# Kernel optimization log

Hardware: AMD Instinct MI355X
Metric: run time of the kernel (lower is better)

Reference implementation:

```python
import jax, jax.numpy as jnp
import numpy as np

D_STATE = 16
D_CONV = 4
EXPAND = 2
GROUPS = 8
EPS = 1e-5


def _layernorm(x, w, b):
    m = x.mean(-1, keepdims=True)
    v = x.var(-1, keepdims=True)
    return (x - m) * jax.lax.rsqrt(v + EPS) * w + b


def _groupnorm(x, w, b):
    B, C = x.shape[:2]
    sp = x.shape[2:]
    xg = x.reshape(B, GROUPS, C // GROUPS, -1)
    m = xg.mean(axis=(2, 3), keepdims=True)
    v = xg.var(axis=(2, 3), keepdims=True)
    xg = (xg - m) * jax.lax.rsqrt(v + EPS)
    x = xg.reshape((B, C) + sp)
    shp = (1, C) + (1,) * len(sp)
    return x * w.reshape(shp) + b.reshape(shp)


def _mamba(xn, in_w, conv_w, conv_b, xp_w, dt_w, dt_b, A_log, Dp, out_w):
    # xn: [B, L, C]
    B, L, C = xn.shape
    di = in_w.shape[0] // 2
    rank = dt_w.shape[1]
    N = D_STATE
    xz = xn @ in_w.T                              # [B, L, 2*di]
    xi, z = xz[..., :di], xz[..., di:]
    # causal depthwise conv1d along L (pad left d_conv-1, truncate to L)
    xc = jnp.moveaxis(xi, 1, 2)                   # [B, di, L]
    xpd = jnp.pad(xc, ((0, 0), (0, 0), (D_CONV - 1, 0)))
    conv = conv_b[None, :, None]
    for k in range(D_CONV):
        conv = conv + conv_w[None, :, k, None] * xpd[:, :, k:k + L]
    u = jnp.moveaxis(jax.nn.silu(conv), 1, 2)     # [B, L, di]
    dbl = u @ xp_w.T                              # [B, L, rank+2N]
    dt = dbl[..., :rank]
    Bm = dbl[..., rank:rank + N]
    Cm = dbl[..., rank + N:]
    delta = jax.nn.softplus(dt @ dt_w.T + dt_b)   # [B, L, di]
    A = -jnp.exp(A_log)                           # [di, N]
    dA = jnp.exp(delta[..., None] * A)            # [B, L, di, N]
    dBu = delta[..., None] * Bm[:, :, None, :] * u[..., None]

    def comb(e1, e2):
        a1, b1 = e1
        a2, b2 = e2
        return a1 * a2, a2 * b1 + b2

    _, h = jax.lax.associative_scan(comb, (dA, dBu), axis=1)  # h_t = dA_t*h_{t-1} + dBu_t
    y = jnp.einsum('bldn,bln->bld', h, Cm) + u * Dp
    y = y * jax.nn.silu(z)
    return y @ out_w.T


def _mamba_layer(x, p):
    B, C = x.shape[:2]
    img = x.shape[2:]
    L = int(np.prod(img))
    xf = jnp.moveaxis(x.reshape(B, C, L), 1, 2)   # [B, L, C]
    xn = _layernorm(xf, p['ln_w'], p['ln_b'])
    xm = _mamba(xn, p['in_w'], p['conv_w'], p['conv_b'], p['xp_w'],
                p['dt_w'], p['dt_b'], p['A_log'], p['Dp'], p['out_w'])
    xm = xm + p['skip'] * xf
    xm = _layernorm(xm, p['ln_w'], p['ln_b'])     # same norm params reused, as in source
    y = xm @ p['proj_w'].T + p['proj_b']
    return jnp.moveaxis(y, 1, 2).reshape((B, C) + img)


def setup_inputs() -> dict:
    key = jax.random.key(0)
    B, C = 2, 48
    img = (16, 32, 32)
    di = EXPAND * C
    rank = -(-C // 16)
    ks = iter(jax.random.split(key, 64))

    def nrm(shape, scale):
        return jax.random.normal(next(ks), shape, jnp.float32) * scale

    inp = {'x': jax.random.normal(next(ks), (B, C) + img, jnp.float32)}
    inp['gn1_w'] = jnp.ones(C); inp['gn1_b'] = jnp.zeros(C)
    inp['gn2_w'] = jnp.ones(C); inp['gn2_b'] = jnp.zeros(C)
    for i in (1, 2):
        inp[f'ln{i}_w'] = jnp.ones(C); inp[f'ln{i}_b'] = jnp.zeros(C)
        inp[f'in_w{i}'] = nrm((2 * di, C), C ** -0.5)
        inp[f'conv_w{i}'] = nrm((di, D_CONV), D_CONV ** -0.5)
        inp[f'conv_b{i}'] = jnp.zeros(di)
        inp[f'xp_w{i}'] = nrm((rank + 2 * D_STATE, di), di ** -0.5)
        inp[f'dt_w{i}'] = nrm((di, rank), rank ** -0.5)
        inp[f'dt_b{i}'] = nrm((di,), 0.1) - 4.0  # softplus -> small positive dt
        inp[f'A_log{i}'] = jnp.log(jnp.tile(jnp.arange(1, D_STATE + 1, dtype=jnp.float32), (di, 1)))
        inp[f'D{i}'] = jnp.ones(di)
        inp[f'out_w{i}'] = nrm((C, di), di ** -0.5)
        inp[f'proj_w{i}'] = nrm((C, C), C ** -0.5)
        inp[f'proj_b{i}'] = jnp.zeros(C)
        inp[f'skip{i}'] = jnp.ones(1)
    return inp


def reference(x, gn1_w, gn1_b, gn2_w, gn2_b,
              ln1_w, ln1_b, in_w1, conv_w1, conv_b1, xp_w1, dt_w1, dt_b1, A_log1, D1, out_w1, proj_w1, proj_b1, skip1,
              ln2_w, ln2_b, in_w2, conv_w2, conv_b2, xp_w2, dt_w2, dt_b2, A_log2, D2, out_w2, proj_w2, proj_b2, skip2):
    p1 = dict(ln_w=ln1_w, ln_b=ln1_b, in_w=in_w1, conv_w=conv_w1, conv_b=conv_b1, xp_w=xp_w1,
              dt_w=dt_w1, dt_b=dt_b1, A_log=A_log1, Dp=D1, out_w=out_w1, proj_w=proj_w1,
              proj_b=proj_b1, skip=skip1)
    p2 = dict(ln_w=ln2_w, ln_b=ln2_b, in_w=in_w2, conv_w=conv_w2, conv_b=conv_b2, xp_w=xp_w2,
              dt_w=dt_w2, dt_b=dt_b2, A_log=A_log2, Dp=D2, out_w=out_w2, proj_w=proj_w2,
              proj_b=proj_b2, skip=skip2)
    identity = x
    h = jax.nn.relu(_groupnorm(x, gn1_w, gn1_b))
    h = _mamba_layer(h, p1)
    h = jax.nn.relu(_groupnorm(h, gn2_w, gn2_b))
    h = _mamba_layer(h, p2)
    return h + identity
```

## Files before the change

### kernel.cpp

```cpp
#include <hip/hip_runtime.h>
#include <hip/hip_bf16.h>

#define LCH   48
#define DI    96
#define LSEQ  16384
#define NB    2
#define NPOS  (NB*LSEQ)
#define NSTATE 16
#define CPG   6
#define EPS   1e-5f
#define NC    128
#define CL    128
#define NCHAIN (NB*DI*NSTATE)
#define TS    32
#define TSS   36
#define LOG2E 1.442695040888963f

typedef __hip_bfloat16 bf16;

__device__ __forceinline__ float LDW(const void* p, size_t i, bool f32){
    return f32 ? ((const float*)p)[i] : __bfloat162float(((const bf16*)p)[i]);
}

__device__ __forceinline__ float bf2f(unsigned short h){
    union { unsigned int i; float f; } u; u.i = ((unsigned int)h) << 16; return u.f;
}

__device__ __forceinline__ float4 LDW4(const void* p, size_t i4, bool f32){
    if (f32) return ((const float4*)p)[i4];
    ushort4 v = ((const ushort4*)p)[i4];
    return make_float4(bf2f(v.x), bf2f(v.y), bf2f(v.z), bf2f(v.w));
}

__device__ __forceinline__ float row16_sum(float p){
    union { float f; int i; } u, v;
    u.f = p; v.i = __builtin_amdgcn_mov_dpp(u.i, 0x111, 0xf, 0xf, true); p += v.f;
    u.f = p; v.i = __builtin_amdgcn_mov_dpp(u.i, 0x112, 0xf, 0xf, true); p += v.f;
    u.f = p; v.i = __builtin_amdgcn_mov_dpp(u.i, 0x114, 0xf, 0xf, true); p += v.f;
    u.f = p; v.i = __builtin_amdgcn_mov_dpp(u.i, 0x118, 0xf, 0xf, true); p += v.f;
    return p;
}

__global__ void k_flag(const void* gnw, int* flag, float* __restrict__ acc1, float* __restrict__ acc2){
    int t = threadIdx.x;
    if (t == 0){
        const unsigned short* g = (const unsigned short*)gnw;
        flag[0] = (g[0] == 0x3F80) ? 0 : 1;
    }
    if (t < 32){ acc1[t] = 0.f; acc2[t] = 0.f; }
}

__global__ void k_gnpart_x(const void* __restrict__ x, const int* Fg, float* __restrict__ acc){
    const bool f32 = Fg[0];
    int bg = blockIdx.x >> 4, sl = blockIdx.x & 15;
    int b = bg >> 3, g = bg & 7;
    int tid = threadIdx.x;
    float s = 0.f, q = 0.f;
    for (int c = 0; c < CPG; ++c){
        size_t base = (size_t)(b*LCH + g*CPG + c)*LSEQ + sl*1024;
        float4 v = LDW4(x, base/4 + tid, f32);
        s += v.x; q += v.x*v.x;
        s += v.y; q += v.y*v.y;
        s += v.z; q += v.z*v.z;
        s += v.w; q += v.w*v.w;
    }
    __shared__ float ss[256], sq[256];
    ss[tid] = s; sq[tid] = q; __syncthreads();
    for (int st = 128; st > 0; st >>= 1){
        if (tid < st){ ss[tid] += ss[tid+st]; sq[tid] += sq[tid+st]; }
        __syncthreads();
    }
    if (tid == 0){
        atomicAdd(&acc[bg*2],   ss[0]);
        atomicAdd(&acc[bg*2+1], sq[0]);
    }
}

template<int SRC>
__global__ void k_prepin(const void* __restrict__ src, const int* Fg, const float* __restrict__ acc,
                         const void* gnw, const void* gnb, const void* lnw, const void* lnb,
                         const void* __restrict__ inw,
                         float* __restrict__ xf, float* __restrict__ xi, float* __restrict__ z){
    const bool f32 = Fg[0];
    __shared__ float wl[96*52];
    __shared__ float xl[32*52];
    __shared__ float fl[32*52];
    __shared__ float sst[32];
    int tid = threadIdx.x;
    int part = blockIdx.x & 1;
    int pos0 = (blockIdx.x >> 1)*32;
    int b = pos0 >> 14, l0 = pos0 & (LSEQ-1);
    if (tid < 16){
        float mean = acc[tid*2] / (float)(CPG*LSEQ);
        float var  = acc[tid*2+1] / (float)(CPG*LSEQ) - mean*mean;
        sst[tid*2]   = mean;
        sst[tid*2+1] = rsqrtf(var + EPS);
    }
    for (int i = tid; i < 96*12; i += 256){
        int o = i/12, k4 = i - o*12;
        ((float4*)wl)[o*13+k4] = LDW4(inw, (size_t)part*1152 + i, f32);
    }
    if (SRC == 0){
        for (int i = tid; i < 48*32; i += 256){
            int c = i >> 5, p = i & 31;
            xl[p*52+c] = LDW(src, (size_t)(b*LCH+c)*LSEQ + l0 + p, f32);
        }
    } else {
        const float4* ms4 = (const float4*)src;
        for (int i = tid; i < 32*12; i += 256){
            int p = i/12, c4 = i - p*12;
            ((float4*)xl)[p*13+c4] = ms4[(size_t)pos0*12 + i];
        }
    }
    __syncthreads();
    {
        int row = tid >> 3, q = tid & 7;
        float* rrow = xl + row*52;
        float* frow = fl + row*52;
        float gmean = sst[(b*8+q)*2], grs = sst[(b*8+q)*2+1];
        float vv[6];
        float s = 0.f, qq = 0.f;
        #pragma unroll
        for (int j = 0; j < 6; ++j){
            int c = q*6 + j;
            float v = rrow[c];
            v = (v - gmean)*grs*LDW(gnw,c,f32) + LDW(gnb,c,f32);
            v = fmaxf(v, 0.f);
            vv[j] = v; frow[c] = v; s += v; qq += v*v;
        }
        s  += __shfl_xor(s, 1);  qq += __shfl_xor(qq, 1);
        s  += __shfl_xor(s, 2);  qq += __shfl_xor(qq, 2);
        s  += __shfl_xor(s, 4);  qq += __shfl_xor(qq, 4);
        float mean = s / (float)LCH;
        float rs = rsqrtf(qq/(float)LCH - mean*mean + EPS);
        #pragma unroll
        for (int j = 0; j < 6; ++j){
            int c = q*6 + j;
            rrow[c] = (vv[j]-mean)*rs*LDW(lnw,c,f32) + LDW(lnb,c,f32);
        }
    }
    __syncthreads();
    if (part == 0){
        float4* xf4 = (float4*)xf;
        const float4* fl4 = (const float4*)fl;
        for (int i = tid; i < 32*12; i += 256){
            int p = i/12, c4 = i - p*12;
            xf4[(size_t)pos0*12 + i] = fl4[p*13+c4];
        }
    }
    float* dst = part ? z : xi;
    int o  = tid & 31;
    int pg = tid >> 5;
    const float4* wl4 = (const float4*)wl;
    const float4* xl4 = (const float4*)xl;
    float a0[4] = {0.f,0.f,0.f,0.f};
    float a1[4] = {0.f,0.f,0.f,0.f};
    float a2[4] = {0.f,0.f,0.f,0.f};
    #pragma unroll
    for (int k4 = 0; k4 < 12; ++k4){
        float4 w0 = wl4[ o     *13 + k4];
        float4 w1 = wl4[(o+32)*13 + k4];
        float4 w2 = wl4[(o+64)*13 + k4];
        #pragma unroll
        for (int q = 0; q < 4; ++q){
            float4 xv = xl4[(pg*4+q)*13 + k4];
            a0[q] += xv.x*w0.x; a0[q] += xv.y*w0.y; a0[q] += xv.z*w0.z; a0[q] += xv.w*w0.w;
            a1[q] += xv.x*w1.x; a1[q] += xv.y*w1.y; a1[q] += xv.z*w1.z; a1[q] += xv.w*w1.w;
            a2[q] += xv.x*w2.x; a2[q] += xv.y*w2.y; a2[q] += xv.z*w2.z; a2[q] += xv.w*w2.w;
        }
    }
    #pragma unroll
    for (int q = 0; q < 4; ++q){
        size_t pos = (size_t)(pos0 + pg*4 + q);
        dst[pos*DI + o     ] = a0[q];
        dst[pos*DI + o + 32] = a1[q];
        dst[pos*DI + o + 64] = a2[q];
    }
}

__global__ void k_convdbl(const float* __restrict__ xi, const void* cw, const void* cb,
                          const void* __restrict__ xpw, const void* dtw, const void* dtb,
                          const int* Fg, float* __restrict__ u_g, float* __restrict__ B2,
                          float* __restrict__ C2, float* __restrict__ delta_g){
    const bool f32 = Fg[0];
    __shared__ float xil[35*100];
    __shared__ float wbc[32*100];
    __shared__ float wdt[3*100];
    __shared__ float cwl[96*4];
    __shared__ float cbl[96];
    __shared__ float dtwl[96*3];
    __shared__ float dtbl[96];
    __shared__ float dtl[32*3];
    int tid = threadIdx.x;
    int pos0 = blockIdx.x*32;
    int l0 = pos0 & (LSEQ-1);

    for (int i = tid; i < 32*24; i += 256){
        int o = i/24, k4 = i - o*24;
        int row = (o & 1) ? (19 + (o>>1)) : (3 + (o>>1));
        ((float4*)wbc)[o*25 + k4] = LDW4(xpw, (size_t)row*24 + k4, f32);
    }
    if (tid < 72){
        int o = tid/24, k4 = tid - o*24;
        ((float4*)wdt)[o*25 + k4] = LDW4(xpw, (size_t)o*24 + k4, f32);
    }
    for (int i = tid; i < 96*4; i += 256) cwl[i] = LDW(cw, i, f32);
    if (tid < 96) cbl[tid] = LDW(cb, tid, f32);
    for (int i = tid; i < 96*3; i += 256) dtwl[i] = LDW(dtw, i, f32);
    if (tid >= 128 && tid < 224) dtbl[tid-128] = LDW(dtb, tid-128, f32);
    {
        float4* xv = (float4*)xil;
        const float4* gx = (const float4*)xi;
        for (int i = tid; i < 35*24; i += 256){
            int p = i/24, k4 = i - p*24;
            float4 v = make_float4(0.f, 0.f, 0.f, 0.f);
            if (l0 + p - 3 >= 0) v = gx[(size_t)(pos0-3+p)*24 + k4];
            xv[p*25 + k4] = v;
        }
    }
    __syncthreads();

    float uu[12];
    #pragma unroll
    for (int r = 0; r < 12; ++r){
        int i = tid + 256*r;
        int j = i/96, d = i - j*96;
        float4 cw4 = ((const float4*)cwl)[d];
        float acc = cbl[d];
        acc += cw4.x*xil[(j+0)*100+d];
        acc += cw4.y*xil[(j+1)*100+d];
        acc += cw4.z*xil[(j+2)*100+d];
        acc += cw4.w*xil[(j+3)*100+d];
        uu[r] = acc / (1.f + __expf(-acc));
    }
    __syncthreads();

    #pragma unroll
    for (int r = 0; r < 12; ++r){
        int i = tid + 256*r;
        int j = i/96, d = i - j*96;
        xil[j*100+d] = uu[r];
        u_g[(size_t)pos0*DI + i] = uu[r];
    }
    __syncthreads();

    {
        int o  = tid & 31;
        int pg = ((tid>>6)<<1) | ((tid>>5)&1);
        const float4* ulv = (const float4*)xil;
        const float4* wv  = (const float4*)wbc;
        float a0=0.f, a1=0.f, a2=0.f, a3=0.f;
        #pragma unroll 4
        for (int k4 = 0; k4 < 24; ++k4){
            float4 u0 = ulv[(pg*4+0)*25 + k4];
            float4 u1 = ulv[(pg*4+1)*25 + k4];
            float4 u2 = ulv[(pg*4+2)*25 + k4];
            float4 u3 = ulv[(pg*4+3)*25 + k4];
            float4 w  = wv[o*25 + k4];
            a0 += u0.x*w.x; a0 += u0.y*w.y; a0 += u0.z*w.z; a0 += u0.w*w.w;
            a1 += u1.x*w.x; a1 += u1.y*w.y; a1 += u1.z*w.z; a1 += u1.w*w.w;
            a2 += u2.x*w.x; a2 += u2.y*w.y; a2 += u2.z*w.z; a2 += u2.w*w.w;
            a3 += u3.x*w.x; a3 += u3.y*w.y; a3 += u3.z*w.z; a3 += u3.w*w.w;
        }
        int nn = o >> 1;
        float* dst = (o & 1) ? C2 : B2;
        size_t pb = (size_t)(pos0 + pg*4);
        dst[(pb+0)*16 + nn] = a0;
        dst[(pb+1)*16 + nn] = a1;
        dst[(pb+2)*16 + nn] = a2;
        dst[(pb+3)*16 + nn] = a3;
    }
    if (tid < 96){
        int o = tid >> 5;
        int p = tid & 31;
        const float4* ulv = (const float4*)xil;
        const float4* wv  = (const float4*)wdt;
        float a = 0.f;
        #pragma unroll 4
        for (int k4 = 0; k4 < 24; ++k4){
            float4 uv = ulv[p*25 + k4];
            float4 w  = wv[o*25 + k4];
            a += uv.x*w.x; a += uv.y*w.y; a += uv.z*w.z; a += uv.w*w.w;
        }
        dtl[p*3+o] = a;
    }
    __syncthreads();

    for (int i = tid; i < 32*96; i += 256){
        int p = i/96, d = i - p*96;
        float acc = dtbl[d];
        #pragma unroll
        for (int r = 0; r < 3; ++r) acc += dtl[p*3+r]*dtwl[d*3+r];
        float sp = (acc > 20.f) ? acc : log1pf(__expf(acc));
        delta_g[(size_t)pos0*DI + i] = sp;
    }
}

__global__ void k_scanA(const float* __restrict__ delta, const float* __restrict__ u,
                        const float* __restrict__ B2, const void* Alog, const int* Fg,
                        float* __restrict__ Pb, float* __restrict__ Sb){
    const bool f32 = Fg[0];
    __shared__ float dls[2][16*TSS];
    __shared__ float uus[2][16*TSS];
    __shared__ float bbs[2][16*TSS];
    int tid = threadIdx.x;
    int t = blockIdx.x*256 + tid;
    int n = tid & 15;
    int sg0 = blockIdx.x*16;
    int cb2 = sg0/96;
    int d0 = sg0 - cb2*96;
    int b = cb2 & 1, chunk = cb2 >> 1;
    int dloc = tid >> 4;
    int d = d0 + dloc;
    float An = -__expf(LDW(Alog, d*16+n, f32)) * LOG2E;
    float P = 1.f, S = 0.f;
    int base = b*LSEQ + chunk*CL;
    int si0 = tid >> 4, sj = tid & 15;
    int si1 = si0 + 16;
    float pd0, pd1, pu0, pu1, pb0, pb1;
    auto fetch = [&](int tb){
        pd0 = delta[(size_t)(tb+si0)*DI + d0 + sj];
        pu0 = u    [(size_t)(tb+si0)*DI + d0 + sj];
        pb0 = B2   [(size_t)(tb+si0)*16 + sj];
        pd1 = delta[(size_t)(tb+si1)*DI + d0 + sj];
        pu1 = u    [(size_t)(tb+si1)*DI + d0 + sj];
        pb1 = B2   [(size_t)(tb+si1)*16 + sj];
    };
    auto store = [&](int bs){
        dls[bs][sj*TSS+si0] = pd0; dls[bs][sj*TSS+si1] = pd1;
        uus[bs][sj*TSS+si0] = pu0; uus[bs][sj*TSS+si1] = pu1;
        bbs[bs][sj*TSS+si0] = pb0; bbs[bs][sj*TSS+si1] = pb1;
    };
    fetch(base); store(0);
    __syncthreads();
    for (int tile = 0; tile < CL/TS; ++tile){
        int cur = tile & 1;
        if (tile+1 < CL/TS) fetch(base + (tile+1)*TS);
        #pragma unroll
        for (int i4 = 0; i4 < TS/4; ++i4){
            float4 dl4 = *(const float4*)&dls[cur][dloc*TSS + i4*4];
            float4 uu4 = *(const float4*)&uus[cur][dloc*TSS + i4*4];
            float4 bn4 = *(const float4*)&bbs[cur][n   *TSS + i4*4];
            float a;
            a = exp2f(dl4.x*An); P *= a; S = a*S + dl4.x*bn4.x*uu4.x;
            a = exp2f(dl4.y*An); P *= a; S = a*S + dl4.y*bn4.y*uu4.y;
            a = exp2f(dl4.z*An); P *= a; S = a*S + dl4.z*bn4.z*uu4.z;
            a = exp2f(dl4.w*An); P *= a; S = a*S + dl4.w*bn4.w*uu4.w;
        }
        if (tile+1 < CL/TS) store(1-cur);
        __syncthreads();
    }
    Pb[t] = P; Sb[t] = S;
}

__global__ void k_scanB(const float* __restrict__ Pb, const float* __restrict__ Sb,
                        float* __restrict__ carry){
    int ch = blockIdx.x*blockDim.x + threadIdx.x;
    float c = 0.f;
    for (int cb = 0; cb < NC; cb += 8){
        float P[8], S[8];
        #pragma unroll
        for (int j = 0; j < 8; ++j){
            P[j] = Pb[(size_t)(cb+j)*NCHAIN + ch];
            S[j] = Sb[(size_t)(cb+j)*NCHAIN + ch];
        }
        #pragma unroll
        for (int j = 0; j < 8; ++j){
            carry[(size_t)(cb+j)*NCHAIN + ch] = c;
            c = S[j] + P[j]*c;
        }
    }
}

__global__ void k_scanC(const float* __restrict__ delta, const float* __restrict__ u,
                        const float* __restrict__ B2, const float* __restrict__ C2,
                        const float* __restrict__ carry, const void* Alog, const void* Dp,
                        const int* Fg, float* __restrict__ y){
    const bool f32 = Fg[0];
    __shared__ float dls[2][16*TSS];
    __shared__ float uus[2][16*TSS];
    __shared__ float bbs[2][16*TSS];
    __shared__ float ccs[2][16*TSS];
    int tid = threadIdx.x;
    int n = tid & 15;
    int sg0 = blockIdx.x*16;
    int cb2 = sg0/96;
    int d0 = sg0 - cb2*96;
    int b = cb2 & 1, chunk = cb2 >> 1;
    int dloc = tid >> 4;
    int d = d0 + dloc;
    float An = -__expf(LDW(Alog, d*16+n, f32)) * LOG2E;
    float Dpd = LDW(Dp, d, f32);
    float h = carry[chunk*NCHAIN + (b*DI+d)*NSTATE + n];
    int base = b*LSEQ + chunk*CL;
    int si0 = tid >> 4, sj = tid & 15;
    int si1 = si0 + 16;
    float pd0, pd1, pu0, pu1, pb0, pb1, pc0, pc1;
    auto fetch = [&](int tb){
        pd0 = delta[(size_t)(tb+si0)*DI + d0 + sj];
        pu0 = u    [(size_t)(tb+si0)*DI + d0 + sj];
        pb0 = B2   [(size_t)(tb+si0)*16 + sj];
        pc0 = C2   [(size_t)(tb+si0)*16 + sj];
        pd1 = delta[(size_t)(tb+si1)*DI + d0 + sj];
        pu1 = u    [(size_t)(tb+si1)*DI + d0 + sj];
        pb1 = B2   [(size_t)(tb+si1)*16 + sj];
        pc1 = C2   [(size_t)(tb+si1)*16 + sj];
    };
    auto store = [&](int bs){
        dls[bs][sj*TSS+si0] = pd0; dls[bs][sj*TSS+si1] = pd1;
        uus[bs][sj*TSS+si0] = pu0; uus[bs][sj*TSS+si1] = pu1;
        bbs[bs][sj*TSS+si0] = pb0; bbs[bs][sj*TSS+si1] = pb1;
        ccs[bs][sj*TSS+si0] = pc0; ccs[bs][sj*TSS+si1] = pc1;
    };
    fetch(base); store(0);
    __syncthreads();
    for (int tile = 0; tile < CL/TS; ++tile){
        int cur = tile & 1;
        int tb = base + tile*TS;
        if (tile+1 < CL/TS) fetch(base + (tile+1)*TS);
        #pragma unroll
        for (int i4 = 0; i4 < TS/4; ++i4){
            float4 dl4 = *(const float4*)&dls[cur][dloc*TSS + i4*4];
            float4 uu4 = *(const float4*)&uus[cur][dloc*TSS + i4*4];
            float4 bn4 = *(const float4*)&bbs[cur][n   *TSS + i4*4];
            float4 cn4 = *(const float4*)&ccs[cur][n   *TSS + i4*4];
            float a, p;
            a = exp2f(dl4.x*An); h = a*h + dl4.x*bn4.x*uu4.x;
            p = row16_sum(h*cn4.x);
            if (n == 15) y[(size_t)(tb+i4*4+0)*DI + d] = p + uu4.x*Dpd;
            a = exp2f(dl4.y*An); h = a*h + dl4.y*bn4.y*uu4.y;
            p = row16_sum(h*cn4.y);
            if (n == 15) y[(size_t)(tb+i4*4+1)*DI + d] = p + uu4.y*Dpd;
            a = exp2f(dl4.z*An); h = a*h + dl4.z*bn4.z*uu4.z;
            p = row16_sum(h*cn4.z);
            if (n == 15) y[(size_t)(tb+i4*4+2)*DI + d] = p + uu4.z*Dpd;
            a = exp2f(dl4.w*An); h = a*h + dl4.w*bn4.w*uu4.w;
            p = row16_sum(h*cn4.w);
            if (n == 15) y[(size_t)(tb+i4*4+3)*DI + d] = p + uu4.w*Dpd;
        }
        if (tile+1 < CL/TS) store(1-cur);
        __syncthreads();
    }
}

__global__ void k_outproj(const float* __restrict__ psum, const void* __restrict__ outw,
                          const void* skipv, const int* Fg,
                          const float* __restrict__ zx,
                          const float* __restrict__ xf, float* __restrict__ xm){
    const bool f32 = Fg[0];
    __shared__ float wl[48*100];
    __shared__ float yl[32*100];
    int tid = threadIdx.x;
    int pos0 = blockIdx.x*32;
    for (int i = tid; i < 48*24; i += 256){
        int o = i/24, k4 = i - o*24;
        ((float4*)wl)[o*25+k4] = LDW4(outw, i, f32);
    }
    {
        const float4* ps4 = (const float4*)psum;
        const float4* zz4 = (const float4*)zx;
        for (int i = tid; i < 32*24; i += 256){
            int p = i/24, k4 = i - p*24;
            float4 pv = ps4[(size_t)pos0*24 + i];
            float4 zv = zz4[(size_t)pos0*24 + i];
            float4 y;
            y.x = pv.x * (zv.x / (1.f + __expf(-zv.x)));
            y.y = pv.y * (zv.y / (1.f + __expf(-zv.y)));
            y.z = pv.z * (zv.z / (1.f + __expf(-zv.z)));
            y.w = pv.w * (zv.w / (1.f + __expf(-zv.w)));
            ((float4*)yl)[p*25+k4] = y;
        }
    }
    __syncthreads();
    float sk = LDW(skipv, 0, f32);
    int o16 = tid & 15;
    int pg  = tid >> 4;
    const float4* wl4 = (const float4*)wl;
    const float4* yl4 = (const float4*)yl;
    float a[3][2] = {{0.f,0.f},{0.f,0.f},{0.f,0.f}};
    #pragma unroll 4
    for (int k4 = 0; k4 < 24; ++k4){
        float4 w0 = wl4[ o16     *25+k4];
        float4 w1 = wl4[(o16+16)*25+k4];
        float4 w2 = wl4[(o16+32)*25+k4];
        float4 y0 = yl4[(pg*2+0)*25+k4];
        float4 y1 = yl4[(pg*2+1)*25+k4];
        a[0][0] += y0.x*w0.x; a[0][0] += y0.y*w0.y; a[0][0] += y0.z*w0.z; a[0][0] += y0.w*w0.w;
        a[0][1] += y1.x*w0.x; a[0][1] += y1.y*w0.y; a[0][1] += y1.z*w0.z; a[0][1] += y1.w*w0.w;
        a[1][0] += y0.x*w1.x; a[1][0] += y0.y*w1.y; a[1][0] += y0.z*w1.z; a[1][0] += y0.w*w1.w;
        a[1][1] += y1.x*w1.x; a[1][1] += y1.y*w1.y; a[1][1] += y1.z*w1.z; a[1][1] += y1.w*w1.w;
        a[2][0] += y0.x*w2.x; a[2][0] += y0.y*w2.y; a[2][0] += y0.z*w2.z; a[2][0] += y0.w*w2.w;
        a[2][1] += y1.x*w2.x; a[2][1] += y1.y*w2.y; a[2][1] += y1.z*w2.z; a[2][1] += y1.w*w2.w;
    }
    #pragma unroll
    for (int r = 0; r < 3; ++r){
        #pragma unroll
        for (int q = 0; q < 2; ++q){
            size_t oi = (size_t)(pos0+pg*2+q)*LCH + o16 + r*16;
            xm[oi] = a[r][q] + sk*xf[oi];
        }
    }
}

template<int FIN>
__global__ void k_lnproj(const float* __restrict__ xm, const void* lnw, const void* lnb,
                         const void* __restrict__ pw, const void* pb, const int* Fg,
                         const void* __restrict__ xres, float* __restrict__ mout,
                         float* __restrict__ acc2, void* __restrict__ outp){
    const bool f32 = Fg[0];
    __shared__ float wp[48*52];
    __shared__ float xl[32*52];
    __shared__ float ol[32*49];
    __shared__ float gs[48], gq[48];
    int tid = threadIdx.x;
    int pos0 = blockIdx.x*32;
    if (FIN == 0 && tid < 48){ gs[tid] = 0.f; gq[tid] = 0.f; }
    for (int i = tid; i < 48*12; i += 256){
        int o = i/12, k4 = i - o*12;
        ((float4*)wp)[o*13+k4] = LDW4(pw, i, f32);
    }
    {
        const float4* xm4 = (const float4*)xm;
        for (int i = tid; i < 32*12; i += 256){
            int p = i/12, c4 = i - p*12;
            ((float4*)xl)[p*13+c4] = xm4[(size_t)pos0*12 + i];
        }
    }
    __syncthreads();
    {
        int row = tid >> 3, q = tid & 7;
        float* rrow = xl + row*52;
        float vv[6];
        float s = 0.f, qq = 0.f;
        #pragma unroll
        for (int j = 0; j < 6; ++j){
            float v = rrow[q*6+j];
            vv[j] = v; s += v; qq += v*v;
        }
        s  += __shfl_xor(s, 1);  qq += __shfl_xor(qq, 1);
        s  += __shfl_xor(s, 2);  qq += __shfl_xor(qq, 2);
        s  += __shfl_xor(s, 4);  qq += __shfl_xor(qq, 4);
        float mean = s / (float)LCH;
        float rs = rsqrtf(qq/(float)LCH - mean*mean + EPS);
        #pragma unroll
        for (int j = 0; j < 6; ++j){
            int c = q*6 + j;
            rrow[c] = (vv[j]-mean)*rs*LDW(lnw,c,f32) + LDW(lnb,c,f32);
        }
    }
    __syncthreads();
    int o16 = tid & 15;
    int pg  = tid >> 4;
    float b0 = LDW(pb, o16,      f32);
    float b1 = LDW(pb, o16 + 16, f32);
    float b2 = LDW(pb, o16 + 32, f32);
    const float4* wp4 = (const float4*)wp;
    const float4* xl4 = (const float4*)xl;
    float a[3][2] = {{b0,b0},{b1,b1},{b2,b2}};
    #pragma unroll 4
    for (int k4 = 0; k4 < 12; ++k4){
        float4 w0 = wp4[ o16     *13+k4];
        float4 w1 = wp4[(o16+16)*13+k4];
        float4 w2 = wp4[(o16+32)*13+k4];
        float4 x0 = xl4[(pg*2+0)*13+k4];
        float4 x1 = xl4[(pg*2+1)*13+k4];
        a[0][0] += x0.x*w0.x; a[0][0] += x0.y*w0.y; a[0][0] += x0.z*w0.z; a[0][0] += x0.w*w0.w;
        a[0][1] += x1.x*w0.x; a[0][1] += x1.y*w0.y; a[0][1] += x1.z*w0.z; a[0][1] += x1.w*w0.w;
        a[1][0] += x0.x*w1.x; a[1][0] += x0.y*w1.y; a[1][0] += x0.z*w1.z; a[1][0] += x0.w*w1.w;
        a[1][1] += x1.x*w1.x; a[1][1] += x1.y*w1.y; a[1][1] += x1.z*w1.z; a[1][1] += x1.w*w1.w;
        a[2][0] += x0.x*w2.x; a[2][0] += x0.y*w2.y; a[2][0] += x0.z*w2.z; a[2][0] += x0.w*w2.w;
        a[2][1] += x1.x*w2.x; a[2][1] += x1.y*w2.y; a[2][1] += x1.z*w2.z; a[2][1] += x1.w*w2.w;
    }
    if (FIN == 0){
        float sl[3] = {0.f,0.f,0.f}, ql[3] = {0.f,0.f,0.f};
        #pragma unroll
        for (int r = 0; r < 3; ++r){
            #pragma unroll
            for (int q = 0; q < 2; ++q){
                float v = a[r][q];
                mout[(size_t)(pos0+pg*2+q)*LCH + o16 + r*16] = v;
                sl[r] += v; ql[r] += v*v;
            }
        }
        #pragma unroll
        for (int r = 0; r < 3; ++r){
            float s = sl[r], q2 = ql[r];
            s  += __shfl_xor(s, 16);  q2 += __shfl_xor(q2, 16);
            s  += __shfl_xor(s, 32);  q2 += __shfl_xor(q2, 32);
            if ((tid & 63) < 16){
                atomicAdd(&gs[o16 + r*16], s);
                atomicAdd(&gq[o16 + r*16], q2);
            }
        }
        __syncthreads();
        if (tid < 8){
            int b = pos0 >> 14;
            float s = 0.f, q = 0.f;
            #pragma unroll
            for (int c = 0; c < CPG; ++c){ s += gs[tid*CPG+c]; q += gq[tid*CPG+c]; }
            atomicAdd(&acc2[(b*8+tid)*2],   s);
            atomicAdd(&acc2[(b*8+tid)*2+1], q);
        }
    } else {
        #pragma unroll
        for (int r = 0; r < 3; ++r){
            #pragma unroll
            for (int q = 0; q < 2; ++q)
                ol[(pg*2+q)*49 + o16 + r*16] = a[r][q];
        }
        __syncthreads();
        int b = pos0 >> 14, l0 = pos0 & (LSEQ-1);
        for (int i = tid; i < 48*32; i += 256){
            int c = i >> 5, p = i & 31;
            size_t gi = (size_t)(b*LCH+c)*LSEQ + l0 + p;
            float v = ol[p*49+c] + LDW(xres, gi, f32);
            if (f32) ((float*)outp)[gi] = v;
            else     ((bf16*)outp)[gi] = __float2bfloat16(v);
        }
    }
}

extern "C" void kernel_launch(void* const* d_in, const int* in_sizes, int n_in,
                              void* d_out, int out_size, void* d_ws, size_t ws_size,
                              hipStream_t stream){
    const void* x = d_in[0];
    auto W = [&](int i){ return (const void*)d_in[i]; };

    float* ws = (float*)d_ws;
    size_t off = 0;
    int*   flag  = (int*)ws;  off += 16;
    float* acc1  = ws + off;  off += 32;
    float* acc2  = ws + off;  off += 32;
    float* xf    = ws + off;  off += (size_t)NPOS*LCH;
    float* xi    = ws + off;  off += (size_t)NPOS*DI;
    float* zb    = ws + off;  off += (size_t)NPOS*DI;
    float* ub    = ws + off;  off += (size_t)NPOS*DI;
    float* B2    = ws + off;  off += (size_t)NPOS*16;
    float* C2    = ws + off;  off += (size_t)NPOS*16;
    float* Pb    = ws + off;  off += (size_t)NC*NCHAIN;
    float* Sb    = ws + off;  off += (size_t)NC*NCHAIN;
    float* carry = ws + off;  off += (size_t)NC*NCHAIN;
    float* delta = ws + off;  off += (size_t)NPOS*DI;
    float* mbuf  = ws + off;  off += (size_t)NPOS*LCH;
    float* ybuf  = xi;
    float* xmbuf = delta;

    k_flag<<<1, 64, 0, stream>>>(W(1), flag, acc1, acc2);

    k_gnpart_x<<<256, 256, 0, stream>>>(x, flag, acc1);
    k_prepin<0><<<2*NPOS/32, 256, 0, stream>>>(x, flag, acc1, W(1), W(2), W(5), W(6), W(7), xf, xi, zb);
    k_convdbl<<<NPOS/32, 256, 0, stream>>>(xi, W(8), W(9), W(10), W(11), W(12), flag, ub, B2, C2, delta);
    k_scanA<<<NC*NCHAIN/256, 256, 0, stream>>>(delta, ub, B2, W(13), flag, Pb, Sb);
    k_scanB<<<NCHAIN/256, 256, 0, stream>>>(Pb, Sb, carry);
    k_scanC<<<NC*NCHAIN/256, 256, 0, stream>>>(delta, ub, B2, C2, carry, W(13), W(14), flag, ybuf);
    k_outproj<<<NPOS/32, 256, 0, stream>>>(ybuf, W(15), W(18), flag, zb, xf, xmbuf);
    k_lnproj<0><<<NPOS/32, 256, 0, stream>>>(xmbuf, W(5), W(6), W(16), W(17), flag, nullptr, mbuf, acc2, nullptr);

    k_prepin<1><<<2*NPOS/32, 256, 0, stream>>>(mbuf, flag, acc2, W(3), W(4), W(19), W(20), W(21), xf, xi, zb);
    k_convdbl<<<NPOS/32, 256, 0, stream>>>(xi, W(22), W(23), W(24), W(25), W(26), flag, ub, B2, C2, delta);
    k_scanA<<<NC*NCHAIN/256, 256, 0, stream>>>(delta, ub, B2, W(27), flag, Pb, Sb);
    k_scanB<<<NCHAIN/256, 256, 0, stream>>>(Pb, Sb, carry);
    k_scanC<<<NC*NCHAIN/256, 256, 0, stream>>>(delta, ub, B2, C2, carry, W(27), W(28), flag, ybuf);
    k_outproj<<<NPOS/32, 256, 0, stream>>>(ybuf, W(29), W(32), flag, zb, xf, xmbuf);
    k_lnproj<1><<<NPOS/32, 256, 0, stream>>>(xmbuf, W(19), W(20), W(30), W(31), flag, x, nullptr, nullptr, d_out);
}
```

Baseline: 413.1 us.

## Pre-transpose projection weights once and read them from global memory in matmul kernels

A new prep kernel transposes the in, out and proj weights for both layers into k-major fp32 buffers in the workspace. The prepin, outproj and lnproj kernels no longer stage weights into shared memory per block. They read the transposed weights directly from global/L2 with coalesced float4 loads and use 16-position tiles instead of 32. prepin now computes both xi and z in one block, so the duplicated groupnorm/layernorm work across two blocks goes away. In exchange, every block issues more global weight reads and there are twice as many blocks, each doing less reuse per weight load.

```diff
diff --git a/kernel.cpp b/kernel.cpp
--- a/kernel.cpp
+++ b/kernel.cpp
@@ -50,6 +50,26 @@
     if (t < 32){ acc1[t] = 0.f; acc2[t] = 0.f; }
 }
 
+__global__ void k_wprep(const void* in1, const void* ow1, const void* pw1,
+                        const void* in2, const void* ow2, const void* pw2,
+                        const int* Fg, float* __restrict__ wT1, float* __restrict__ wT2){
+    const bool f32 = Fg[0];
+    int gid = blockIdx.x*256 + threadIdx.x;
+    if (gid >= 2*4032) return;
+    int layer = gid / 4032, r = gid - layer*4032;
+    float4* wT = (float4*)(layer ? wT2 : wT1);
+    if (r < 2304){
+        int k4 = r/192, row = r - k4*192;
+        wT[r] = LDW4(layer ? in2 : in1, (size_t)row*12 + k4, f32);
+    } else if (r < 3456){
+        int rr = r - 2304, k4 = rr/48, row = rr - k4*48;
+        wT[r] = LDW4(layer ? ow2 : ow1, (size_t)row*24 + k4, f32);
+    } else {
+        int rr = r - 3456, k4 = rr/48, row = rr - k4*48;
+        wT[r] = LDW4(layer ? pw2 : pw1, (size_t)row*12 + k4, f32);
+    }
+}
+
 __global__ void k_gnpart_x(const void* __restrict__ x, const int* Fg, float* __restrict__ acc){
     const bool f32 = Fg[0];
     int bg = blockIdx.x >> 4, sl = blockIdx.x & 15;
@@ -79,16 +99,14 @@
 template<int SRC>
 __global__ void k_prepin(const void* __restrict__ src, const int* Fg, const float* __restrict__ acc,
                          const void* gnw, const void* gnb, const void* lnw, const void* lnb,
-                         const void* __restrict__ inw,
+                         const float* __restrict__ wT,
                          float* __restrict__ xf, float* __restrict__ xi, float* __restrict__ z){
     const bool f32 = Fg[0];
-    __shared__ float wl[96*52];
-    __shared__ float xl[32*52];
-    __shared__ float fl[32*52];
+    __shared__ float xl[16*52];
+    __shared__ float fl[16*52];
     __shared__ float sst[32];
     int tid = threadIdx.x;
-    int part = blockIdx.x & 1;
-    int pos0 = (blockIdx.x >> 1)*32;
+    int pos0 = blockIdx.x*16;
     int b = pos0 >> 14, l0 = pos0 & (LSEQ-1);
     if (tid < 16){
         float mean = acc[tid*2] / (float)(CPG*LSEQ);
@@ -96,24 +114,20 @@
         sst[tid*2]   = mean;
         sst[tid*2+1] = rsqrtf(var + EPS);
     }
-    for (int i = tid; i < 96*12; i += 256){
-        int o = i/12, k4 = i - o*12;
-        ((float4*)wl)[o*13+k4] = LDW4(inw, (size_t)part*1152 + i, f32);
-    }
     if (SRC == 0){
-        for (int i = tid; i < 48*32; i += 256){
-            int c = i >> 5, p = i & 31;
+        for (int i = tid; i < 48*16; i += 256){
+            int c = i >> 4, p = i & 15;
             xl[p*52+c] = LDW(src, (size_t)(b*LCH+c)*LSEQ + l0 + p, f32);
         }
     } else {
         const float4* ms4 = (const float4*)src;
-        for (int i = tid; i < 32*12; i += 256){
+        for (int i = tid; i < 16*12; i += 256){
             int p = i/12, c4 = i - p*12;
             ((float4*)xl)[p*13+c4] = ms4[(size_t)pos0*12 + i];
         }
     }
     __syncthreads();
-    {
+    if (tid < 128){
         int row = tid >> 3, q = tid & 7;
         float* rrow = xl + row*52;
         float* frow = fl + row*52;
@@ -140,41 +154,39 @@
         }
     }
     __syncthreads();
-    if (part == 0){
+    {
         float4* xf4 = (float4*)xf;
         const float4* fl4 = (const float4*)fl;
-        for (int i = tid; i < 32*12; i += 256){
+        for (int i = tid; i < 16*12; i += 256){
             int p = i/12, c4 = i - p*12;
             xf4[(size_t)pos0*12 + i] = fl4[p*13+c4];
         }
     }
-    float* dst = part ? z : xi;
     int o  = tid & 31;
-    int pg = tid >> 5;
-    const float4* wl4 = (const float4*)wl;
+    int pq = tid >> 5;
+    const float4* wT4 = (const float4*)wT;
     const float4* xl4 = (const float4*)xl;
-    float a0[4] = {0.f,0.f,0.f,0.f};
-    float a1[4] = {0.f,0.f,0.f,0.f};
-    float a2[4] = {0.f,0.f,0.f,0.f};
+    float a[6][2] = {{0.f,0.f},{0.f,0.f},{0.f,0.f},{0.f,0.f},{0.f,0.f},{0.f,0.f}};
     #pragma unroll
     for (int k4 = 0; k4 < 12; ++k4){
-        float4 w0 = wl4[ o     *13 + k4];
-        float4 w1 = wl4[(o+32)*13 + k4];
-        float4 w2 = wl4[(o+64)*13 + k4];
-        #pragma unroll
-        for (int q = 0; q < 4; ++q){
-            float4 xv = xl4[(pg*4+q)*13 + k4];
-            a0[q] += xv.x*w0.x; a0[q] += xv.y*w0.y; a0[q] += xv.z*w0.z; a0[q] += xv.w*w0.w;
-            a1[q] += xv.x*w1.x; a1[q] += xv.y*w1.y; a1[q] += xv.z*w1.z; a1[q] += xv.w*w1.w;
-            a2[q] += xv.x*w2.x; a2[q] += xv.y*w2.y; a2[q] += xv.z*w2.z; a2[q] += xv.w*w2.w;
+        float4 x0 = xl4[(pq*2+0)*13 + k4];
+        float4 x1 = xl4[(pq*2+1)*13 + k4];
+        #pragma unroll
+        for (int r = 0; r < 6; ++r){
+            float4 w = wT4[k4*192 + o + 32*r];
+            a[r][0] += x0.x*w.x; a[r][0] += x0.y*w.y; a[r][0] += x0.z*w.z; a[r][0] += x0.w*w.w;
+            a[r][1] += x1.x*w.x; a[r][1] += x1.y*w.y; a[r][1] += x1.z*w.z; a[r][1] += x1.w*w.w;
         }
     }
     #pragma unroll
-    for (int q = 0; q < 4; ++q){
-        size_t pos = (size_t)(pos0 + pg*4 + q);
-        dst[pos*DI + o     ] = a0[q];
-        dst[pos*DI + o + 32] = a1[q];
-        dst[pos*DI + o + 64] = a2[q];
+    for (int q = 0; q < 2; ++q){
+        size_t pos = (size_t)(pos0 + pq*2 + q);
+        xi[pos*DI + o     ] = a[0][q];
+        xi[pos*DI + o + 32] = a[1][q];
+        xi[pos*DI + o + 64] = a[2][q];
+        z [pos*DI + o     ] = a[3][q];
+        z [pos*DI + o + 32] = a[4][q];
+        z [pos*DI + o + 64] = a[5][q];
     }
 }
 
@@ -443,23 +455,18 @@
     }
 }
 
-__global__ void k_outproj(const float* __restrict__ psum, const void* __restrict__ outw,
+__global__ void k_outproj(const float* __restrict__ psum, const float* __restrict__ owT,
                           const void* skipv, const int* Fg,
                           const float* __restrict__ zx,
                           const float* __restrict__ xf, float* __restrict__ xm){
     const bool f32 = Fg[0];
-    __shared__ float wl[48*100];
-    __shared__ float yl[32*100];
+    __shared__ float yl[16*100];
     int tid = threadIdx.x;
-    int pos0 = blockIdx.x*32;
-    for (int i = tid; i < 48*24; i += 256){
-        int o = i/24, k4 = i - o*24;
-        ((float4*)wl)[o*25+k4] = LDW4(outw, i, f32);
-    }
+    int pos0 = blockIdx.x*16;
     {
         const float4* ps4 = (const float4*)psum;
         const float4* zz4 = (const float4*)zx;
-        for (int i = tid; i < 32*24; i += 256){
+        for (int i = tid; i < 16*24; i += 256){
             int p = i/24, k4 = i - p*24;
             float4 pv = ps4[(size_t)pos0*24 + i];
             float4 zv = zz4[(size_t)pos0*24 + i];
@@ -474,60 +481,47 @@
     __syncthreads();
     float sk = LDW(skipv, 0, f32);
     int o16 = tid & 15;
-    int pg  = tid >> 4;
-    const float4* wl4 = (const float4*)wl;
+    int p   = tid >> 4;
+    const float4* wT4 = (const float4*)owT;
     const float4* yl4 = (const float4*)yl;
-    float a[3][2] = {{0.f,0.f},{0.f,0.f},{0.f,0.f}};
+    float a0 = 0.f, a1 = 0.f, a2 = 0.f;
     #pragma unroll 4
     for (int k4 = 0; k4 < 24; ++k4){
-        float4 w0 = wl4[ o16     *25+k4];
-        float4 w1 = wl4[(o16+16)*25+k4];
-        float4 w2 = wl4[(o16+32)*25+k4];
-        float4 y0 = yl4[(pg*2+0)*25+k4];
-        float4 y1 = yl4[(pg*2+1)*25+k4];
-        a[0][0] += y0.x*w0.x; a[0][0] += y0.y*w0.y; a[0][0] += y0.z*w0.z; a[0][0] += y0.w*w0.w;
-        a[0][1] += y1.x*w0.x; a[0][1] += y1.y*w0.y; a[0][1] += y1.z*w0.z; a[0][1] += y1.w*w0.w;
-        a[1][0] += y0.x*w1.x; a[1][0] += y0.y*w1.y; a[1][0] += y0.z*w1.z; a[1][0] += y0.w*w1.w;
-        a[1][1] += y1.x*w1.x; a[1][1] += y1.y*w1.y; a[1][1] += y1.z*w1.z; a[1][1] += y1.w*w1.w;
-        a[2][0] += y0.x*w2.x; a[2][0] += y0.y*w2.y; a[2][0] += y0.z*w2.z; a[2][0] += y0.w*w2.w;
-        a[2][1] += y1.x*w2.x; a[2][1] += y1.y*w2.y; a[2][1] += y1.z*w2.z; a[2][1] += y1.w*w2.w;
-    }
-    #pragma unroll
-    for (int r = 0; r < 3; ++r){
-        #pragma unroll
-        for (int q = 0; q < 2; ++q){
-            size_t oi = (size_t)(pos0+pg*2+q)*LCH + o16 + r*16;
-            xm[oi] = a[r][q] + sk*xf[oi];
-        }
-    }
+        float4 y = yl4[p*25+k4];
+        float4 w0 = wT4[k4*48 + o16];
+        float4 w1 = wT4[k4*48 + o16+16];
+        float4 w2 = wT4[k4*48 + o16+32];
+        a0 += y.x*w0.x; a0 += y.y*w0.y; a0 += y.z*w0.z; a0 += y.w*w0.w;
+        a1 += y.x*w1.x; a1 += y.y*w1.y; a1 += y.z*w1.z; a1 += y.w*w1.w;
+        a2 += y.x*w2.x; a2 += y.y*w2.y; a2 += y.z*w2.z; a2 += y.w*w2.w;
+    }
+    size_t ob = (size_t)(pos0+p)*LCH + o16;
+    xm[ob     ] = a0 + sk*xf[ob     ];
+    xm[ob + 16] = a1 + sk*xf[ob + 16];
+    xm[ob + 32] = a2 + sk*xf[ob + 32];
 }
 
 template<int FIN>
 __global__ void k_lnproj(const float* __restrict__ xm, const void* lnw, const void* lnb,
-                         const void* __restrict__ pw, const void* pb, const int* Fg,
+                         const float* __restrict__ pwT, const void* pb, const int* Fg,
                          const void* __restrict__ xres, float* __restrict__ mout,
                          float* __restrict__ acc2, void* __restrict__ outp){
     const bool f32 = Fg[0];
-    __shared__ float wp[48*52];
-    __shared__ float xl[32*52];
-    __shared__ float ol[32*49];
+    __shared__ float xl[16*52];
+    __shared__ float ol[16*49];
     __shared__ float gs[48], gq[48];
     int tid = threadIdx.x;
-    int pos0 = blockIdx.x*32;
+    int pos0 = blockIdx.x*16;
     if (FIN == 0 && tid < 48){ gs[tid] = 0.f; gq[tid] = 0.f; }
-    for (int i = tid; i < 48*12; i += 256){
-        int o = i/12, k4 = i - o*12;
-        ((float4*)wp)[o*13+k4] = LDW4(pw, i, f32);
-    }
     {
         const float4* xm4 = (const float4*)xm;
-        for (int i = tid; i < 32*12; i += 256){
+        for (int i = tid; i < 16*12; i += 256){
             int p = i/12, c4 = i - p*12;
             ((float4*)xl)[p*13+c4] = xm4[(size_t)pos0*12 + i];
         }
     }
     __syncthreads();
-    {
+    if (tid < 128){
         int row = tid >> 3, q = tid & 7;
         float* rrow = xl + row*52;
         float vv[6];
@@ -550,41 +544,31 @@
     }
     __syncthreads();
     int o16 = tid & 15;
-    int pg  = tid >> 4;
-    float b0 = LDW(pb, o16,      f32);
-    float b1 = LDW(pb, o16 + 16, f32);
-    float b2 = LDW(pb, o16 + 32, f32);
-    const float4* wp4 = (const float4*)wp;
+    int p   = tid >> 4;
+    float a0 = LDW(pb, o16,      f32);
+    float a1 = LDW(pb, o16 + 16, f32);
+    float a2 = LDW(pb, o16 + 32, f32);
+    const float4* wT4 = (const float4*)pwT;
     const float4* xl4 = (const float4*)xl;
-    float a[3][2] = {{b0,b0},{b1,b1},{b2,b2}};
     #pragma unroll 4
     for (int k4 = 0; k4 < 12; ++k4){
-        float4 w0 = wp4[ o16     *13+k4];
-        float4 w1 = wp4[(o16+16)*13+k4];
-        float4 w2 = wp4[(o16+32)*13+k4];
-        float4 x0 = xl4[(pg*2+0)*13+k4];
-        float4 x1 = xl4[(pg*2+1)*13+k4];
-        a[0][0] += x0.x*w0.x; a[0][0] += x0.y*w0.y; a[0][0] += x0.z*w0.z; a[0][0] += x0.w*w0.w;
-        a[0][1] += x1.x*w0.x; a[0][1] += x1.y*w0.y; a[0][1] += x1.z*w0.z; a[0][1] += x1.w*w0.w;
-        a[1][0] += x0.x*w1.x; a[1][0] += x0.y*w1.y; a[1][0] += x0.z*w1.z; a[1][0] += x0.w*w1.w;
-        a[1][1] += x1.x*w1.x; a[1][1] += x1.y*w1.y; a[1][1] += x1.z*w1.z; a[1][1] += x1.w*w1.w;
-        a[2][0] += x0.x*w2.x; a[2][0] += x0.y*w2.y; a[2][0] += x0.z*w2.z; a[2][0] += x0.w*w2.w;
-        a[2][1] += x1.x*w2.x; a[2][1] += x1.y*w2.y; a[2][1] += x1.z*w2.z; a[2][1] += x1.w*w2.w;
+        float4 x = xl4[p*13+k4];
+        float4 w0 = wT4[k4*48 + o16];
+        float4 w1 = wT4[k4*48 + o16+16];
+        float4 w2 = wT4[k4*48 + o16+32];
+        a0 += x.x*w0.x; a0 += x.y*w0.y; a0 += x.z*w0.z; a0 += x.w*w0.w;
+        a1 += x.x*w1.x; a1 += x.y*w1.y; a1 += x.z*w1.z; a1 += x.w*w1.w;
+        a2 += x.x*w2.x; a2 += x.y*w2.y; a2 += x.z*w2.z; a2 += x.w*w2.w;
     }
     if (FIN == 0){
-        float sl[3] = {0.f,0.f,0.f}, ql[3] = {0.f,0.f,0.f};
+        size_t ob = (size_t)(pos0+p)*LCH + o16;
+        mout[ob     ] = a0;
+        mout[ob + 16] = a1;
+        mout[ob + 32] = a2;
+        float sv[3] = {a0, a1, a2}, qv[3] = {a0*a0, a1*a1, a2*a2};
         #pragma unroll
         for (int r = 0; r < 3; ++r){
-            #pragma unroll
-            for (int q = 0; q < 2; ++q){
-                float v = a[r][q];
-                mout[(size_t)(pos0+pg*2+q)*LCH + o16 + r*16] = v;
-                sl[r] += v; ql[r] += v*v;
-            }
-        }
-        #pragma unroll
-        for (int r = 0; r < 3; ++r){
-            float s = sl[r], q2 = ql[r];
+            float s = sv[r], q2 = qv[r];
             s  += __shfl_xor(s, 16);  q2 += __shfl_xor(q2, 16);
             s  += __shfl_xor(s, 32);  q2 += __shfl_xor(q2, 32);
             if ((tid & 63) < 16){
@@ -602,18 +586,15 @@
             atomicAdd(&acc2[(b*8+tid)*2+1], q);
         }
     } else {
-        #pragma unroll
-        for (int r = 0; r < 3; ++r){
-            #pragma unroll
-            for (int q = 0; q < 2; ++q)
-                ol[(pg*2+q)*49 + o16 + r*16] = a[r][q];
-        }
+        ol[p*49 + o16     ] = a0;
+        ol[p*49 + o16 + 16] = a1;
+        ol[p*49 + o16 + 32] = a2;
         __syncthreads();
         int b = pos0 >> 14, l0 = pos0 & (LSEQ-1);
-        for (int i = tid; i < 48*32; i += 256){
-            int c = i >> 5, p = i & 31;
-            size_t gi = (size_t)(b*LCH+c)*LSEQ + l0 + p;
-            float v = ol[p*49+c] + LDW(xres, gi, f32);
+        for (int i = tid; i < 48*16; i += 256){
+            int c = i >> 4, p2 = i & 15;
+            size_t gi = (size_t)(b*LCH+c)*LSEQ + l0 + p2;
+            float v = ol[p2*49+c] + LDW(xres, gi, f32);
             if (f32) ((float*)outp)[gi] = v;
             else     ((bf16*)outp)[gi] = __float2bfloat16(v);
         }
@@ -631,6 +612,8 @@
     int*   flag  = (int*)ws;  off += 16;
     float* acc1  = ws + off;  off += 32;
     float* acc2  = ws + off;  off += 32;
+    float* wT1   = ws + off;  off += 16128;
+    float* wT2   = ws + off;  off += 16128;
     float* xf    = ws + off;  off += (size_t)NPOS*LCH;
     float* xi    = ws + off;  off += (size_t)NPOS*DI;
     float* zb    = ws + off;  off += (size_t)NPOS*DI;
@@ -646,21 +629,22 @@
     float* xmbuf = delta;
 
     k_flag<<<1, 64, 0, stream>>>(W(1), flag, acc1, acc2);
+    k_wprep<<<32, 256, 0, stream>>>(W(7), W(15), W(16), W(21), W(29), W(30), flag, wT1, wT2);
 
     k_gnpart_x<<<256, 256, 0, stream>>>(x, flag, acc1);
-    k_prepin<0><<<2*NPOS/32, 256, 0, stream>>>(x, flag, acc1, W(1), W(2), W(5), W(6), W(7), xf, xi, zb);
+    k_prepin<0><<<NPOS/16, 256, 0, stream>>>(x, flag, acc1, W(1), W(2), W(5), W(6), wT1, xf, xi, zb);
     k_convdbl<<<NPOS/32, 256, 0, stream>>>(xi, W(8), W(9), W(10), W(11), W(12), flag, ub, B2, C2, delta);
     k_scanA<<<NC*NCHAIN/256, 256, 0, stream>>>(delta, ub, B2, W(13), flag, Pb, Sb);
     k_scanB<<<NCHAIN/256, 256, 0, stream>>>(Pb, Sb, carry);
     k_scanC<<<NC*NCHAIN/256, 256, 0, stream>>>(delta, ub, B2, C2, carry, W(13), W(14), flag, ybuf);
-    k_outproj<<<NPOS/32, 256, 0, stream>>>(ybuf, W(15), W(18), flag, zb, xf, xmbuf);
-    k_lnproj<0><<<NPOS/32, 256, 0, stream>>>(xmbuf, W(5), W(6), W(16), W(17), flag, nullptr, mbuf, acc2, nullptr);
-
-    k_prepin<1><<<2*NPOS/32, 256, 0, stream>>>(mbuf, flag, acc2, W(3), W(4), W(19), W(20), W(21), xf, xi, zb);
+    k_outproj<<<NPOS/16, 256, 0, stream>>>(ybuf, wT1 + 9216, W(18), flag, zb, xf, xmbuf);
+    k_lnproj<0><<<NPOS/16, 256, 0, stream>>>(xmbuf, W(5), W(6), wT1 + 13824, W(17), flag, nullptr, mbuf, acc2, nullptr);
+
+    k_prepin<1><<<NPOS/16, 256, 0, stream>>>(mbuf, flag, acc2, W(3), W(4), W(19), W(20), wT2, xf, xi, zb);
     k_convdbl<<<NPOS/32, 256, 0, stream>>>(xi, W(22), W(23), W(24), W(25), W(26), flag, ub, B2, C2, delta);
     k_scanA<<<NC*NCHAIN/256, 256, 0, stream>>>(delta, ub, B2, W(27), flag, Pb, Sb);
     k_scanB<<<NCHAIN/256, 256, 0, stream>>>(Pb, Sb, carry);
     k_scanC<<<NC*NCHAIN/256, 256, 0, stream>>>(delta, ub, B2, C2, carry, W(27), W(28), flag, ybuf);
-    k_outproj<<<NPOS/32, 256, 0, stream>>>(ybuf, W(29), W(32), flag, zb, xf, xmbuf);
-    k_lnproj<1><<<NPOS/32, 256, 0, stream>>>(xmbuf, W(19), W(20), W(30), W(31), flag, x, nullptr, nullptr, d_out);
-}
+    k_outproj<<<NPOS/16, 256, 0, stream>>>(ybuf, wT2 + 9216, W(32), flag, zb, xf, xmbuf);
+    k_lnproj<1><<<NPOS/16, 256, 0, stream>>>(xmbuf, W(19), W(20), wT2 + 13824, W(31), flag, x, nullptr, nullptr, d_out);
+}
```

New measurement: 469.8 us. 1.14x slower.

## Fuse three-phase chunked scan into one cooperative kernel with grid syncs

Applied to the files above, without the earlier changes.

Merges the chunk-local scan, the cross-chunk carry propagation and the output scan into a single cooperative kernel separated by grid-wide syncs. This removes two kernel launches and their inter-kernel gaps per Mamba layer. If the cooperative launch fails, it falls back to the original three kernels. The cost is grid-sync overhead, a 256×8 launch bound that may force register spills, and full-grid residency, since 1536 blocks must fit at 8 per CU.

```diff
diff --git a/kernel.cpp b/kernel.cpp
--- a/kernel.cpp
+++ b/kernel.cpp
@@ -1,5 +1,8 @@
 #include <hip/hip_runtime.h>
 #include <hip/hip_bf16.h>
+#include <hip/hip_cooperative_groups.h>
+
+namespace cg = cooperative_groups;
 
 #define LCH   48
 #define DI    96
@@ -293,6 +296,142 @@
         for (int r = 0; r < 3; ++r) acc += dtl[p*3+r]*dtwl[d*3+r];
         float sp = (acc > 20.f) ? acc : log1pf(__expf(acc));
         delta_g[(size_t)pos0*DI + i] = sp;
+    }
+}
+
+__global__ void __launch_bounds__(256, 8)
+k_scan(const float* __restrict__ delta, const float* __restrict__ u,
+       const float* __restrict__ B2, const float* __restrict__ C2,
+       const void* Alog, const void* Dp, const int* Fg,
+       float* __restrict__ Pb, float* __restrict__ Sb,
+       float* __restrict__ carry, float* __restrict__ y){
+    const bool f32 = Fg[0];
+    __shared__ float dls[2][16*TSS];
+    __shared__ float uus[2][16*TSS];
+    __shared__ float bbs[2][16*TSS];
+    __shared__ float ccs[2][16*TSS];
+    cg::grid_group gg = cg::this_grid();
+    int tid = threadIdx.x;
+    int t = blockIdx.x*256 + tid;
+    int n = tid & 15;
+    int sg0 = blockIdx.x*16;
+    int cb2 = sg0/96;
+    int d0 = sg0 - cb2*96;
+    int b = cb2 & 1, chunk = cb2 >> 1;
+    int dloc = tid >> 4;
+    int d = d0 + dloc;
+    float An = -__expf(LDW(Alog, d*16+n, f32)) * LOG2E;
+    int base = b*LSEQ + chunk*CL;
+    int si0 = tid >> 4, sj = tid & 15;
+    int si1 = si0 + 16;
+
+    {
+        float P = 1.f, S = 0.f;
+        float pd0, pd1, pu0, pu1, pb0, pb1;
+        auto fetch = [&](int tb){
+            pd0 = delta[(size_t)(tb+si0)*DI + d0 + sj];
+            pu0 = u    [(size_t)(tb+si0)*DI + d0 + sj];
+            pb0 = B2   [(size_t)(tb+si0)*16 + sj];
+            pd1 = delta[(size_t)(tb+si1)*DI + d0 + sj];
+            pu1 = u    [(size_t)(tb+si1)*DI + d0 + sj];
+            pb1 = B2   [(size_t)(tb+si1)*16 + sj];
+        };
+        auto store = [&](int bs){
+            dls[bs][sj*TSS+si0] = pd0; dls[bs][sj*TSS+si1] = pd1;
+            uus[bs][sj*TSS+si0] = pu0; uus[bs][sj*TSS+si1] = pu1;
+            bbs[bs][sj*TSS+si0] = pb0; bbs[bs][sj*TSS+si1] = pb1;
+        };
+        fetch(base); store(0);
+        __syncthreads();
+        for (int tile = 0; tile < CL/TS; ++tile){
+            int cur = tile & 1;
+            if (tile+1 < CL/TS) fetch(base + (tile+1)*TS);
+            #pragma unroll
+            for (int i4 = 0; i4 < TS/4; ++i4){
+                float4 dl4 = *(const float4*)&dls[cur][dloc*TSS + i4*4];
+                float4 uu4 = *(const float4*)&uus[cur][dloc*TSS + i4*4];
+                float4 bn4 = *(const float4*)&bbs[cur][n   *TSS + i4*4];
+                float a;
+                a = exp2f(dl4.x*An); P *= a; S = a*S + dl4.x*bn4.x*uu4.x;
+                a = exp2f(dl4.y*An); P *= a; S = a*S + dl4.y*bn4.y*uu4.y;
+                a = exp2f(dl4.z*An); P *= a; S = a*S + dl4.z*bn4.z*uu4.z;
+                a = exp2f(dl4.w*An); P *= a; S = a*S + dl4.w*bn4.w*uu4.w;
+            }
+            if (tile+1 < CL/TS) store(1-cur);
+            __syncthreads();
+        }
+        Pb[t] = P; Sb[t] = S;
+    }
+    gg.sync();
+
+    if (blockIdx.x < NCHAIN/256){
+        int ch = blockIdx.x*256 + tid;
+        float c = 0.f;
+        for (int cb = 0; cb < NC; cb += 8){
+            float P[8], S[8];
+            #pragma unroll
+            for (int j = 0; j < 8; ++j){
+                P[j] = Pb[(size_t)(cb+j)*NCHAIN + ch];
+                S[j] = Sb[(size_t)(cb+j)*NCHAIN + ch];
+            }
+            #pragma unroll
+            for (int j = 0; j < 8; ++j){
+                carry[(size_t)(cb+j)*NCHAIN + ch] = c;
+                c = S[j] + P[j]*c;
+            }
+        }
+    }
+    gg.sync();
+
+    {
+        float Dpd = LDW(Dp, d, f32);
+        float h = carry[chunk*NCHAIN + (b*DI+d)*NSTATE + n];
+        float pd0, pd1, pu0, pu1, pb0, pb1, pc0, pc1;
+        auto fetch = [&](int tb){
+            pd0 = delta[(size_t)(tb+si0)*DI + d0 + sj];
+            pu0 = u    [(size_t)(tb+si0)*DI + d0 + sj];
+            pb0 = B2   [(size_t)(tb+si0)*16 + sj];
+            pc0 = C2   [(size_t)(tb+si0)*16 + sj];
+            pd1 = delta[(size_t)(tb+si1)*DI + d0 + sj];
+            pu1 = u    [(size_t)(tb+si1)*DI + d0 + sj];
+            pb1 = B2   [(size_t)(tb+si1)*16 + sj];
+            pc1 = C2   [(size_t)(tb+si1)*16 + sj];
+        };
+        auto store = [&](int bs){
+            dls[bs][sj*TSS+si0] = pd0; dls[bs][sj*TSS+si1] = pd1;
+            uus[bs][sj*TSS+si0] = pu0; uus[bs][sj*TSS+si1] = pu1;
+            bbs[bs][sj*TSS+si0] = pb0; bbs[bs][sj*TSS+si1] = pb1;
+            ccs[bs][sj*TSS+si0] = pc0; ccs[bs][sj*TSS+si1] = pc1;
+        };
+        fetch(base); store(0);
+        __syncthreads();
+        for (int tile = 0; tile < CL/TS; ++tile){
+            int cur = tile & 1;
+            int tb = base + tile*TS;
+            if (tile+1 < CL/TS) fetch(base + (tile+1)*TS);
+            #pragma unroll
+            for (int i4 = 0; i4 < TS/4; ++i4){
+                float4 dl4 = *(const float4*)&dls[cur][dloc*TSS + i4*4];
+                float4 uu4 = *(const float4*)&uus[cur][dloc*TSS + i4*4];
+                float4 bn4 = *(const float4*)&bbs[cur][n   *TSS + i4*4];
+                float4 cn4 = *(const float4*)&ccs[cur][n   *TSS + i4*4];
+                float a, p;
+                a = exp2f(dl4.x*An); h = a*h + dl4.x*bn4.x*uu4.x;
+                p = row16_sum(h*cn4.x);
+                if (n == 15) y[(size_t)(tb+i4*4+0)*DI + d] = p + uu4.x*Dpd;
+                a = exp2f(dl4.y*An); h = a*h + dl4.y*bn4.y*uu4.y;
+                p = row16_sum(h*cn4.y);
+                if (n == 15) y[(size_t)(tb+i4*4+1)*DI + d] = p + uu4.y*Dpd;
+                a = exp2f(dl4.z*An); h = a*h + dl4.z*bn4.z*uu4.z;
+                p = row16_sum(h*cn4.z);
+                if (n == 15) y[(size_t)(tb+i4*4+2)*DI + d] = p + uu4.z*Dpd;
+                a = exp2f(dl4.w*An); h = a*h + dl4.w*bn4.w*uu4.w;
+                p = row16_sum(h*cn4.w);
+                if (n == 15) y[(size_t)(tb+i4*4+3)*DI + d] = p + uu4.w*Dpd;
+            }
+            if (tile+1 < CL/TS) store(1-cur);
+            __syncthreads();
+        }
     }
 }
 
@@ -645,22 +784,32 @@
     float* ybuf  = xi;
     float* xmbuf = delta;
 
+    auto scan = [&](const void* alog, const void* dp){
+        const void* alogp = alog; const void* dpp = dp;
+        void* args[] = {(void*)&delta, (void*)&ub, (void*)&B2, (void*)&C2,
+                        (void*)&alogp, (void*)&dpp, (void*)&flag,
+                        (void*)&Pb, (void*)&Sb, (void*)&carry, (void*)&ybuf};
+        hipError_t e = hipLaunchCooperativeKernel((void*)k_scan,
+                          dim3(NC*NCHAIN/256), dim3(256), args, 0, stream);
+        if (e != hipSuccess){
+            k_scanA<<<NC*NCHAIN/256, 256, 0, stream>>>(delta, ub, B2, alog, flag, Pb, Sb);
+            k_scanB<<<NCHAIN/256, 256, 0, stream>>>(Pb, Sb, carry);
+            k_scanC<<<NC*NCHAIN/256, 256, 0, stream>>>(delta, ub, B2, C2, carry, alog, dp, flag, ybuf);
+        }
+    };
+
     k_flag<<<1, 64, 0, stream>>>(W(1), flag, acc1, acc2);
 
     k_gnpart_x<<<256, 256, 0, stream>>>(x, flag, acc1);
     k_prepin<0><<<2*NPOS/32, 256, 0, stream>>>(x, flag, acc1, W(1), W(2), W(5), W(6), W(7), xf, xi, zb);
     k_convdbl<<<NPOS/32, 256, 0, stream>>>(xi, W(8), W(9), W(10), W(11), W(12), flag, ub, B2, C2, delta);
-    k_scanA<<<NC*NCHAIN/256, 256, 0, stream>>>(delta, ub, B2, W(13), flag, Pb, Sb);
-    k_scanB<<<NCHAIN/256, 256, 0, stream>>>(Pb, Sb, carry);
-    k_scanC<<<NC*NCHAIN/256, 256, 0, stream>>>(delta, ub, B2, C2, carry, W(13), W(14), flag, ybuf);
+    scan(W(13), W(14));
     k_outproj<<<NPOS/32, 256, 0, stream>>>(ybuf, W(15), W(18), flag, zb, xf, xmbuf);
     k_lnproj<0><<<NPOS/32, 256, 0, stream>>>(xmbuf, W(5), W(6), W(16), W(17), flag, nullptr, mbuf, acc2, nullptr);
 
     k_prepin<1><<<2*NPOS/32, 256, 0, stream>>>(mbuf, flag, acc2, W(3), W(4), W(19), W(20), W(21), xf, xi, zb);
     k_convdbl<<<NPOS/32, 256, 0, stream>>>(xi, W(22), W(23), W(24), W(25), W(26), flag, ub, B2, C2, delta);
-    k_scanA<<<NC*NCHAIN/256, 256, 0, stream>>>(delta, ub, B2, W(27), flag, Pb, Sb);
-    k_scanB<<<NCHAIN/256, 256, 0, stream>>>(Pb, Sb, carry);
-    k_scanC<<<NC*NCHAIN/256, 256, 0, stream>>>(delta, ub, B2, C2, carry, W(27), W(28), flag, ybuf);
+    scan(W(27), W(28));
     k_outproj<<<NPOS/32, 256, 0, stream>>>(ybuf, W(29), W(32), flag, zb, xf, xmbuf);
     k_lnproj<1><<<NPOS/32, 256, 0, stream>>>(xmbuf, W(19), W(20), W(30), W(31), flag, x, nullptr, nullptr, d_out);
 }
```

New measurement: 1.275 ms. 3.09x slower.
